# Kernel optimization log

Hardware: AMD Instinct MI355X
Metric: run time of the kernel (lower is better)

Reference implementation:

```python
import jax, jax.numpy as jnp
import numpy as np

N = 300000        # occupied voxels
G = 128           # voxel grid side
C_IN = 128
C_OUT = 32
TIMES = C_IN // C_OUT
K = 27            # 3^3 kernel offsets


def _build_kernel_map():
    """Sample N unique voxels in a G^3 grid and build the 27-offset neighbor map.
    nbr[k, n] = index of the voxel at coords[n] + offset[k], or N if absent."""
    rng = np.random.default_rng(0)
    lin = rng.choice(G ** 3, size=N, replace=False).astype(np.int64)
    coords = np.stack(np.unravel_index(lin, (G, G, G)), axis=1).astype(np.int64)  # [N,3]
    lookup = np.full(G ** 3, N, dtype=np.int32)
    lookup[lin] = np.arange(N, dtype=np.int32)
    offs = np.stack(np.meshgrid(*[[-1, 0, 1]] * 3, indexing='ij'), axis=-1).reshape(-1, 3)  # [27,3]
    nbr = np.empty((K, N), dtype=np.int32)
    for k, off in enumerate(offs):
        nc = coords + off
        valid = np.all((nc >= 0) & (nc < G), axis=1)
        li = (nc[:, 0] * G + nc[:, 1]) * G + nc[:, 2]
        nbr[k] = np.where(valid, lookup[np.clip(li, 0, G ** 3 - 1)], N)
    return nbr


def setup_inputs() -> dict:
    key = jax.random.key(0)
    k1, k2, k3, k4 = jax.random.split(key, 4)
    feats = jax.random.normal(k1, (N, C_IN), dtype=jnp.float32)
    W0 = jax.random.normal(k2, (K, C_IN, C_IN), dtype=jnp.float32) * 0.05
    W1 = jax.random.normal(k3, (K, C_IN, C_OUT), dtype=jnp.float32) * 0.05
    W2 = jax.random.normal(k4, (K, C_OUT, C_OUT), dtype=jnp.float32) * 0.05
    nbr_idx = jnp.asarray(_build_kernel_map())
    return {"feats": feats, "W0": W0, "W1": W1, "W2": W2, "nbr_idx": nbr_idx}


def sparse_conv(x, W, nbr):
    """Gather-GEMM-accumulate sparse conv: out[n] = sum_k x[nbr[k,n]] @ W[k].
    Missing neighbors (index N) gather a zero row."""
    xp = jnp.concatenate([x, jnp.zeros((1, x.shape[1]), x.dtype)], axis=0)  # [N+1,Cin]
    out0 = jnp.zeros((x.shape[0], W.shape[2]), x.dtype)

    def body(acc, kw):
        idx, Wk = kw
        return acc + xp[idx] @ Wk, None

    out, _ = jax.lax.scan(body, out0, (nbr, W))
    return out


def reference(feats, W0, W1, W2, nbr_idx):
    n = feats.shape[0]
    # mean over channel groups: [N, times, C_out] -> [N, C_out]
    downsampled = jnp.mean(feats.reshape(n, TIMES, C_OUT), axis=1)
    upsampled = jnp.tile(downsampled, (1, TIMES))           # [N, C_in]
    residual = feats - upsampled
    residual = sparse_conv(residual, W0, nbr_idx)           # C_in -> C_in
    residual = sparse_conv(residual, W1, nbr_idx)           # C_in -> C_out
    residual = sparse_conv(residual, W2, nbr_idx)           # C_out -> C_out
    return downsampled + residual
```

## Files before the change

kernel.cpp:

```cpp
#include <hip/hip_runtime.h>

#define DEVINL __device__ __forceinline__

typedef __attribute__((ext_vector_type(8))) __bf16 bf16x8;
typedef __attribute__((ext_vector_type(4))) float f32x4;
typedef __attribute__((ext_vector_type(8))) unsigned short u16x8;

DEVINL unsigned short f2bf(float x) {
  unsigned u = __builtin_bit_cast(unsigned, x);
  u += 0x7FFFu + ((u >> 16) & 1u);
  return (unsigned short)(u >> 16);
}

#define BARRIER() asm volatile("s_barrier" ::: "memory")

template <int N>
DEVINL void waitvm() {
  asm volatile("s_waitcnt vmcnt(%0)" ::"n"(N) : "memory");
}

DEVINL void gload16(const void* g, void* l) {
  __builtin_amdgcn_global_load_lds(
      (const __attribute__((address_space(1))) void*)g,
      (__attribute__((address_space(3))) void*)l, 16, 0, 0);
}

__global__ __launch_bounds__(256) void prep_kernel(
    const float* __restrict__ F, unsigned short* __restrict__ RES,
    float* __restrict__ DS, int n) {
  const int t = threadIdx.x;
  const int row = blockIdx.x * 16 + (t >> 4);
  const int cg = t & 15;
  if (row >= n) return;
  const float4* f4 = (const float4*)(F + (size_t)row * 128 + cg * 8);
  float4 v0 = f4[0], v1 = f4[1];
  float v[8] = {v0.x, v0.y, v0.z, v0.w, v1.x, v1.y, v1.z, v1.w};
  float s[8] = {v0.x, v0.y, v0.z, v0.w, v1.x, v1.y, v1.z, v1.w};
#pragma unroll
  for (int i = 0; i < 8; ++i) s[i] += __shfl_xor(s[i], 4);
#pragma unroll
  for (int i = 0; i < 8; ++i) s[i] += __shfl_xor(s[i], 8);
  u16x8 rb;
#pragma unroll
  for (int i = 0; i < 8; ++i) rb[i] = f2bf(v[i] - 0.25f * s[i]);
  *(u16x8*)(RES + (size_t)row * 128 + cg * 8) = rb;
  if (cg < 4) {
    float4 d0 = {0.25f * s[0], 0.25f * s[1], 0.25f * s[2], 0.25f * s[3]};
    float4 d1 = {0.25f * s[4], 0.25f * s[5], 0.25f * s[6], 0.25f * s[7]};
    float4* dp = (float4*)(DS + (size_t)row * 32 + cg * 8);
    dp[0] = d0;
    dp[1] = d1;
  }
}

template <int CIN, int COUT>
DEVINL void pack_one(const float* __restrict__ W, unsigned short* __restrict__ P, int g) {
  const int n = g % COUT;
  const int t = g / COUT;
  const int q = t & 3;
  const int t2 = t >> 2;
  const int ks = t2 % (CIN / 32);
  const int k = t2 / (CIN / 32);
  const float* src = W + ((size_t)k * CIN + ks * 32 + q * 8) * COUT + n;
  unsigned short* dst = P + (size_t)g * 8;
#pragma unroll
  for (int j = 0; j < 8; ++j) dst[j] = f2bf(src[(size_t)j * COUT]);
}

__global__ __launch_bounds__(256) void pack_kernel(
    const float* __restrict__ W0, const float* __restrict__ W1,
    const float* __restrict__ W2, unsigned short* __restrict__ P0,
    unsigned short* __restrict__ P1, unsigned short* __restrict__ P2) {
  int g = blockIdx.x * 256 + threadIdx.x;
  if (g < 55296)
    pack_one<128, 128>(W0, P0, g);
  else if (g < 69120)
    pack_one<128, 32>(W1, P1, g - 55296);
  else if (g < 72576)
    pack_one<32, 32>(W2, P2, g - 69120);
}

__global__ void zero_tail(unsigned short* a, unsigned short* b, unsigned short* c) {
  int t = threadIdx.x;
  if (t < 128) { a[t] = 0; b[t] = 0; }
  if (t < 32) c[t] = 0;
}

template <int CIN, int COUT, int BK, int BM, int WM, int WN, bool FINAL, int MINB>
__global__ __launch_bounds__(256, MINB) void spconv(
    const unsigned short* __restrict__ X, const unsigned short* __restrict__ Bp,
    const int* __restrict__ nbr, unsigned short* __restrict__ Y,
    float* __restrict__ OUT, const float* __restrict__ DS, int nr) {
  constexpr int H = CIN / BK;
  constexpr int S = 27 * H;
  constexpr int KSL = BK / 32;
  constexpr int WROWS = BM / WM;
  constexpr int WCOLS = COUT / WN;
  constexpr int MF = WROWS / 16;
  constexpr int NF = WCOLS / 16;
  constexpr int CPR = BK / 8;
  constexpr int SWZ = (CPR < 8 ? CPR - 1 : 7);
  constexpr int RB = BK * 2;
  constexpr int APF = BM * CPR / 256;
  constexpr int NB = KSL * NF;

  __shared__ unsigned short As[2][BM * BK];
  __shared__ int IdxS[27 * BM];

  const int tid = threadIdx.x;
  const int lane = tid & 63;
  const int wave = tid >> 6;
  const int wm = wave / WN;
  const int wn = wave % WN;
  const int base = blockIdx.x * BM;
  const int q = lane >> 4;
  const int l16 = lane & 15;

  for (int f = tid; f < 27 * BM; f += 256) {
    int k = f / BM;
    int nn = base + (f % BM);
    IdxS[f] = (nn < nr) ? nbr[(size_t)k * nr + nn] : nr;
  }
  __syncthreads();

  const unsigned short* bbase = Bp + ((size_t)q * COUT + wn * WCOLS + l16) * 8;

  bf16x8 bA[NB], bB[NB];

  auto loadB = [&](bf16x8(&dst)[NB], int s) {
    const int k = s / H;
    const int hh = s % H;
#pragma unroll
    for (int ks = 0; ks < KSL; ++ks)
#pragma unroll
      for (int j = 0; j < NF; ++j) {
        const int ksg = hh * KSL + ks;
        dst[ks * NF + j] = *(const bf16x8*)(
            bbase + ((size_t)k * CIN * COUT) + ((size_t)(ksg * 4) * COUT + j * 16) * 8);
      }
  };

  auto issueA = [&](int s) {
    const int k = s / H;
    const int hh = s % H;
    const int kb = s & 1;
#pragma unroll
    for (int pp = 0; pp < APF; ++pp) {
      int slot = pp * 256 + tid;
      int r = slot / CPR;
      int cc = (slot % CPR) * 16;
      int csw = cc ^ ((r & SWZ) << 4);
      int g = IdxS[k * BM + r];
      gload16(X + (size_t)g * CIN + hh * BK + (csw >> 1),
              (char*)(&As[kb][0]) + slot * 16);
    }
  };

  f32x4 acc[MF][NF] = {};

  auto mfmaStep = [&](int kb, const bf16x8(&bf)[NB]) {
    const char* Ab = (const char*)(&As[kb][0]);
#pragma unroll
    for (int ks = 0; ks < KSL; ++ks) {
      bf16x8 af[MF];
#pragma unroll
      for (int i = 0; i < MF; ++i) {
        int r = wm * WROWS + i * 16 + l16;
        int db = r * RB + (((ks * 64 + q * 16) & (RB - 1)) ^ ((r & SWZ) << 4));
        af[i] = __builtin_bit_cast(bf16x8, *(const uint4*)(Ab + db));
      }
#pragma unroll
      for (int i = 0; i < MF; ++i)
#pragma unroll
        for (int j = 0; j < NF; ++j)
          acc[i][j] = __builtin_amdgcn_mfma_f32_16x16x32_bf16(af[i], bf[ks * NF + j],
                                                              acc[i][j], 0, 0, 0);
    }
  };

  loadB(bA, 0);
  issueA(0);

#pragma unroll 1
  for (int s = 0; s + 1 < S; s += 2) {
    loadB(bB, s + 1);
    issueA(s + 1);
    waitvm<NB + APF>();
    BARRIER();
    mfmaStep(0, bA);
    BARRIER();
    if (s + 2 < S) {
      loadB(bA, s + 2);
      issueA(s + 2);
      waitvm<NB + APF>();
    } else {
      waitvm<0>();
    }
    BARRIER();
    mfmaStep(1, bB);
    BARRIER();
  }
  if constexpr (S & 1) {
    waitvm<0>();
    BARRIER();
    mfmaStep(0, bA);
  }

#pragma unroll
  for (int i = 0; i < MF; ++i)
#pragma unroll
    for (int j = 0; j < NF; ++j)
#pragma unroll
      for (int r = 0; r < 4; ++r) {
        int row = base + wm * WROWS + i * 16 + q * 4 + r;
        int col = wn * WCOLS + j * 16 + l16;
        if (row < nr) {
          float v = acc[i][j][r];
          if constexpr (FINAL)
            OUT[(size_t)row * COUT + col] = v + DS[(size_t)row * COUT + col];
          else
            Y[(size_t)row * COUT + col] = f2bf(v);
        }
      }
}

extern "C" void kernel_launch(void* const* d_in, const int* in_sizes, int n_in,
                              void* d_out, int out_size, void* d_ws, size_t ws_size,
                              hipStream_t stream) {
  const float* feats = (const float*)d_in[0];
  const float* W0 = (const float*)d_in[1];
  const float* W1 = (const float*)d_in[2];
  const float* W2 = (const float*)d_in[3];
  const int* nbr = (const int*)d_in[4];
  const int n = in_sizes[0] / 128;
  float* out = (float*)d_out;

  char* p = (char*)d_ws;
  auto take = [&](size_t bytes) {
    char* r = p;
    p += (bytes + 255) & ~(size_t)255;
    return r;
  };
  unsigned short* resB = (unsigned short*)take((size_t)(n + 1) * 128 * 2);
  unsigned short* y0 = (unsigned short*)take((size_t)(n + 1) * 128 * 2);
  unsigned short* y1 = (unsigned short*)take((size_t)(n + 1) * 32 * 2);
  float* ds = (float*)take((size_t)n * 32 * 4);
  unsigned short* p0 = (unsigned short*)take((size_t)27 * 128 * 128 * 2);
  unsigned short* p1 = (unsigned short*)take((size_t)27 * 128 * 32 * 2);
  unsigned short* p2 = (unsigned short*)take((size_t)27 * 32 * 32 * 2);

  prep_kernel<<<(n + 15) / 16, 256, 0, stream>>>(feats, resB, ds, n);
  pack_kernel<<<284, 256, 0, stream>>>(W0, W1, W2, p0, p1, p2);
  zero_tail<<<1, 128, 0, stream>>>(resB + (size_t)n * 128, y0 + (size_t)n * 128,
                                   y1 + (size_t)n * 32);
  const int gb64 = (n + 63) / 64;
  const int gb128 = (n + 127) / 128;
  spconv<128, 128, 64, 64, 1, 4, false, 4>
      <<<gb64, 256, 0, stream>>>(resB, p0, nbr, y0, nullptr, nullptr, n);
  spconv<128, 32, 64, 64, 4, 1, false, 4>
      <<<gb64, 256, 0, stream>>>(y0, p1, nbr, y1, nullptr, nullptr, n);
  spconv<32, 32, 32, 128, 4, 1, true, 4>
      <<<gb128, 256, 0, stream>>>(y1, p2, nbr, nullptr, out, ds, n);
}
```

Measured before the change: 543.6 us.

## Add configurable prefetch depth for gathered A tiles and retune conv2 tiling

The spconv kernel takes a prefetch-depth parameter PF with PF+1 LDS buffers, so gathered rows can be issued PF steps ahead of the MFMA step that uses them. Out-of-range steps gather from a padded 28th index row that points at the zero row. The first conv now uses PF=2, which deepens gather latency hiding at the cost of more LDS. The second conv moves to 128-row blocks with occupancy hint 3, and it and the third conv keep single-step prefetch.

Result: faster. 519.4 us (-4.5%).

```diff
diff --git a/kernel.cpp b/kernel.cpp
--- a/kernel.cpp
+++ b/kernel.cpp
@@ -86,13 +86,15 @@
   if (t < 32) c[t] = 0;
 }
 
-template <int CIN, int COUT, int BK, int BM, int WM, int WN, bool FINAL, int MINB>
+template <int CIN, int COUT, int BK, int BM, int PF, int WM, int WN, bool FINAL,
+          int MINB>
 __global__ __launch_bounds__(256, MINB) void spconv(
     const unsigned short* __restrict__ X, const unsigned short* __restrict__ Bp,
     const int* __restrict__ nbr, unsigned short* __restrict__ Y,
     float* __restrict__ OUT, const float* __restrict__ DS, int nr) {
   constexpr int H = CIN / BK;
   constexpr int S = 27 * H;
+  constexpr int NBUF = PF + 1;
   constexpr int KSL = BK / 32;
   constexpr int WROWS = BM / WM;
   constexpr int WCOLS = COUT / WN;
@@ -104,8 +106,8 @@
   constexpr int APF = BM * CPR / 256;
   constexpr int NB = KSL * NF;
 
-  __shared__ unsigned short As[2][BM * BK];
-  __shared__ int IdxS[27 * BM];
+  __shared__ unsigned short As[NBUF][BM * BK];
+  __shared__ int IdxS[28 * BM];
 
   const int tid = threadIdx.x;
   const int lane = tid & 63;
@@ -116,10 +118,10 @@
   const int q = lane >> 4;
   const int l16 = lane & 15;
 
-  for (int f = tid; f < 27 * BM; f += 256) {
+  for (int f = tid; f < 28 * BM; f += 256) {
     int k = f / BM;
     int nn = base + (f % BM);
-    IdxS[f] = (nn < nr) ? nbr[(size_t)k * nr + nn] : nr;
+    IdxS[f] = (k < 27 && nn < nr) ? nbr[(size_t)k * nr + nn] : nr;
   }
   __syncthreads();
 
@@ -128,7 +130,8 @@
   bf16x8 bA[NB], bB[NB];
 
   auto loadB = [&](bf16x8(&dst)[NB], int s) {
-    const int k = s / H;
+    const int k0 = s / H;
+    const int k = (k0 > 26) ? 26 : k0;
     const int hh = s % H;
 #pragma unroll
     for (int ks = 0; ks < KSL; ++ks)
@@ -143,7 +146,7 @@
   auto issueA = [&](int s) {
     const int k = s / H;
     const int hh = s % H;
-    const int kb = s & 1;
+    const int kb = s % NBUF;
 #pragma unroll
     for (int pp = 0; pp < APF; ++pp) {
       int slot = pp * 256 + tid;
@@ -178,32 +181,29 @@
     }
   };
 
+  issueA(0);
   loadB(bA, 0);
-  issueA(0);
+  if constexpr (PF >= 2) issueA(1);
 
 #pragma unroll 1
   for (int s = 0; s + 1 < S; s += 2) {
     loadB(bB, s + 1);
-    issueA(s + 1);
-    waitvm<NB + APF>();
-    BARRIER();
-    mfmaStep(0, bA);
-    BARRIER();
-    if (s + 2 < S) {
-      loadB(bA, s + 2);
-      issueA(s + 2);
-      waitvm<NB + APF>();
-    } else {
-      waitvm<0>();
-    }
-    BARRIER();
-    mfmaStep(1, bB);
-    BARRIER();
-  }
+    issueA(s + PF);
+    waitvm<NB + PF * APF>();
+    BARRIER();
+    mfmaStep(s % NBUF, bA);
+    BARRIER();
+    loadB(bA, s + 2);
+    issueA(s + 1 + PF);
+    waitvm<NB + PF * APF>();
+    BARRIER();
+    mfmaStep((s + 1) % NBUF, bB);
+    BARRIER();
+  }
+  waitvm<0>();
   if constexpr (S & 1) {
-    waitvm<0>();
-    BARRIER();
-    mfmaStep(0, bA);
+    BARRIER();
+    mfmaStep((S - 1) % NBUF, bA);
   }
 
 #pragma unroll
@@ -255,10 +255,10 @@
                                    y1 + (size_t)n * 32);
   const int gb64 = (n + 63) / 64;
   const int gb128 = (n + 127) / 128;
-  spconv<128, 128, 64, 64, 1, 4, false, 4>
+  spconv<128, 128, 64, 64, 2, 1, 4, false, 4>
       <<<gb64, 256, 0, stream>>>(resB, p0, nbr, y0, nullptr, nullptr, n);
-  spconv<128, 32, 64, 64, 4, 1, false, 4>
-      <<<gb64, 256, 0, stream>>>(y0, p1, nbr, y1, nullptr, nullptr, n);
-  spconv<32, 32, 32, 128, 4, 1, true, 4>
+  spconv<128, 32, 64, 128, 1, 4, 1, false, 3>
+      <<<gb128, 256, 0, stream>>>(y0, p1, nbr, y1, nullptr, nullptr, n);
+  spconv<32, 32, 32, 128, 1, 4, 1, true, 4>
       <<<gb128, 256, 0, stream>>>(y1, p2, nbr, nullptr, out, ds, n);
 }
```
